# Kernel optimization log

Hardware: AMD Instinct MI355X
Metric: run time of the kernel (lower is better)

## Reference

```python
import jax, jax.numpy as jnp
import numpy as np

D = 768       # GATv2 in/out feats (num_heads=1)
D_OUT = 384   # fc output
K = 51        # round(top_rate * L) = round(0.1 * 512)
EPS = 1e-5    # nn.LayerNorm default eps


def _layer_norm(x, g, b):
    mu = jnp.mean(x, axis=-1, keepdims=True)
    var = jnp.mean((x - mu) ** 2, axis=-1, keepdims=True)
    return (x - mu) / jnp.sqrt(var + EPS) * g + b


def setup_inputs() -> dict:
    key = jax.random.key(0)
    ks = jax.random.split(key, 12)
    B, L = 4, 512
    s = 0.02
    return {
        "hidden_state": jax.random.normal(ks[0], (B, L, D), jnp.float32),
        "attention": jax.random.uniform(ks[1], (B, L, L), jnp.float32),
        # GATv2Conv params (fc_src, fc_dst, attn vector, output bias)
        "W_src": jax.random.normal(ks[2], (D, D), jnp.float32) * s,
        "b_src": jnp.zeros((D,), jnp.float32),
        "W_dst": jax.random.normal(ks[3], (D, D), jnp.float32) * s,
        "b_dst": jnp.zeros((D,), jnp.float32),
        "attn_vec": jax.random.normal(ks[4], (D,), jnp.float32) * s,
        "gat_bias": jnp.zeros((D,), jnp.float32),
        # GlobalAttentionPooling gate_nn: Linear(768, 1)
        "gate_W": jax.random.normal(ks[5], (D, 1), jnp.float32) * s,
        "gate_b": jnp.zeros((1,), jnp.float32),
        # LayerNorm(768)
        "ln_g": jnp.ones((D,), jnp.float32),
        "ln_b": jnp.zeros((D,), jnp.float32),
        # fc: Linear(768, 384)
        "fc_W": jax.random.normal(ks[6], (D, D_OUT), jnp.float32) * s,
        "fc_b": jnp.zeros((D_OUT,), jnp.float32),
        # LayerNorm(384)
        "ln2_g": jnp.ones((D_OUT,), jnp.float32),
        "ln2_b": jnp.zeros((D_OUT,), jnp.float32),
        "mask": jnp.ones((B, L), jnp.int32),  # unused by the original forward
        "type": 0,                              # unused string/type flag
    }


def reference(hidden_state, attention, W_src, b_src, W_dst, b_dst, attn_vec,
              gat_bias, gate_W, gate_b, ln_g, ln_b, fc_W, fc_b, ln2_g, ln2_b,
              mask, type):
    B, L, _ = hidden_state.shape
    # --- topk sparsification: each node i keeps K source neighbors ---
    vals, idx = jax.lax.top_k(attention, K)          # [B, L, K]
    valid = vals > 0.0                                # edges kept by pos_sign filter

    # --- GATv2Conv (num_heads=1, residual=Identity since 768==768) ---
    feat_src = hidden_state @ W_src + b_src           # [B, L, D]
    feat_dst = hidden_state @ W_dst + b_dst           # [B, L, D]
    g = feat_src[jnp.arange(B)[:, None, None], idx]   # [B, L, K, D] gathered src feats
    e = jax.nn.leaky_relu(g + feat_dst[:, :, None, :], 0.2)
    scores = jnp.einsum("blkd,d->blk", e, attn_vec)   # [B, L, K]
    scores = jnp.where(valid, scores, -1e9)           # removed edges masked out
    a = jax.nn.softmax(scores, axis=-1)               # edge_softmax per dst node
    h = jnp.einsum("blk,blkd->bld", a, g)             # weighted scatter-sum
    h = h + hidden_state + gat_bias                   # residual (identity) + bias
    h = jax.nn.leaky_relu(h, 0.01)                    # nn.LeakyReLU activation

    # --- GlobalAttentionPooling: softmax(gate) weighted segment reduce ---
    gate = h @ gate_W + gate_b                        # [B, L, 1]
    p = jax.nn.softmax(gate, axis=1)
    pooled = jnp.sum(p * h, axis=1)                   # [B, D]

    # --- head: fc(dropout(ln(relu(out)))) then ln2 (dropout = eval identity) ---
    out = _layer_norm(jax.nn.relu(pooled), ln_g, ln_b)
    out = out @ fc_W + fc_b
    out = _layer_norm(out, ln2_g, ln2_b)
    return out
```

## Files before the change

### kernel.cpp

```cpp
#include <hip/hip_runtime.h>
#include <math.h>

#define D 768
#define DOUT 384
#define LSEQ 512
#define BATCH 4
#define KTOP 51
#define EPS 1e-5f

typedef unsigned short ushort_t;
typedef __bf16 bf16x8 __attribute__((ext_vector_type(8)));
typedef float f32x4 __attribute__((ext_vector_type(4)));

#define GLOAD16(gp, lp)                                                        \
    __builtin_amdgcn_global_load_lds(                                          \
        (const __attribute__((address_space(1))) unsigned int*)(gp),           \
        (__attribute__((address_space(3))) unsigned int*)(lp), 16, 0, 0)

__device__ __forceinline__ ushort_t f2bf(float f) {
    unsigned int u = __builtin_bit_cast(unsigned int, f);
    u = (u + 0x7FFFu + ((u >> 16) & 1u)) >> 16;
    return (ushort_t)u;
}

__device__ __forceinline__ float bf2f(ushort_t u) {
    unsigned int v = ((unsigned int)u) << 16;
    return __builtin_bit_cast(float, v);
}

__global__ __launch_bounds__(256) void prep_kernel(const float* __restrict__ hidden,
                                                   ushort_t* __restrict__ Ah,
                                                   const float* __restrict__ W0,
                                                   const float* __restrict__ W1,
                                                   ushort_t* __restrict__ WT0,
                                                   ushort_t* __restrict__ WT1,
                                                   float* __restrict__ pooled,
                                                   float* __restrict__ z) {
    __shared__ float tile[32][33];
    const int bid = blockIdx.x;
    const int tid = threadIdx.x;
    if (bid < 1536) {
        const int i = (bid * 256 + tid) * 4;
        const float4 v = *(const float4*)(hidden + i);
        ushort4 o;
        o.x = f2bf(v.x); o.y = f2bf(v.y); o.z = f2bf(v.z); o.w = f2bf(v.w);
        *(ushort4*)(Ah + i) = o;
    } else if (bid < 2688) {
        const int t = bid - 1536;
        const int zz = t / 576;
        const int rem = t - zz * 576;
        const int by = rem / 24, bx = rem - by * 24;
        const float* W = zz ? W1 : W0;
        ushort_t* WT = zz ? WT1 : WT0;
        const int kbase = by * 32;
        const int nbase = bx * 32;
        const int r = tid >> 3, c4 = (tid & 7) * 4;

        const float4 v = *(const float4*)(W + (size_t)(kbase + r) * D + nbase + c4);
        tile[r][c4 + 0] = v.x; tile[r][c4 + 1] = v.y;
        tile[r][c4 + 2] = v.z; tile[r][c4 + 3] = v.w;
        __syncthreads();
        ushort4 o;
        o.x = f2bf(tile[c4 + 0][r]); o.y = f2bf(tile[c4 + 1][r]);
        o.z = f2bf(tile[c4 + 2][r]); o.w = f2bf(tile[c4 + 3][r]);
        *(ushort4*)(WT + (size_t)(nbase + r) * D + kbase + c4) = o;
    } else {
        for (int i = tid; i < BATCH * D; i += 256) pooled[i] = 0.f;
        for (int i = tid; i < BATCH * DOUT; i += 256) z[i] = 0.f;
    }
}

__global__ __launch_bounds__(256) void feat_gemm_kernel(const ushort_t* __restrict__ Ah,
                                                        const ushort_t* __restrict__ WT0,
                                                        const float* __restrict__ b0,
                                                        ushort_t* __restrict__ Csrc_bf,
                                                        const ushort_t* __restrict__ WT1,
                                                        const float* __restrict__ b1,
                                                        float* __restrict__ Cdst) {
    const ushort_t* WT = blockIdx.z ? WT1 : WT0;
    const float* bias = blockIdx.z ? b1 : b0;

    __shared__ ushort_t As[64 * 64];
    __shared__ ushort_t Bs[64 * 64];

    const int tid = threadIdx.x;
    const int lane = tid & 63;
    const int wave = tid >> 6;
    const int quad = lane >> 4;
    const int m15 = lane & 15;
    const int qRow = (wave & 1) * 32;
    const int qCol = (wave >> 1) * 32;

    const int rowBase = blockIdx.y * 64;
    const int colBase = blockIdx.x * 64;

    const int e0 = tid * 8;
    const int r0 = e0 >> 6;
    const int c0 = e0 & 63;
    const int cc = c0 >> 3;
    const int csw = (cc ^ (r0 & 7)) << 3;
    const ushort_t* Abase = Ah + (size_t)rowBase * D;
    const ushort_t* Bbase = WT + (size_t)colBase * D;

    f32x4 acc[2][2] = {};

    for (int kk = 0; kk < D; kk += 64) {
        __syncthreads();
        GLOAD16(Abase + (size_t)r0 * D + kk + csw, &As[e0]);
        GLOAD16(Abase + (size_t)(r0 + 32) * D + kk + csw, &As[e0 + 2048]);
        GLOAD16(Bbase + (size_t)r0 * D + kk + csw, &Bs[e0]);
        GLOAD16(Bbase + (size_t)(r0 + 32) * D + kk + csw, &Bs[e0 + 2048]);
        __syncthreads();

        bf16x8 a[2][2], b[2][2];
#pragma unroll
        for (int i = 0; i < 2; ++i) {
            const int row = qRow + i * 16 + m15;
            const int sw = row & 7;
#pragma unroll
            for (int ks = 0; ks < 2; ++ks)
                a[i][ks] = *(const bf16x8*)&As[row * 64 + ((((ks << 2) + quad) ^ sw) << 3)];
        }
#pragma unroll
        for (int j = 0; j < 2; ++j) {
            const int row = qCol + j * 16 + m15;
            const int sw = row & 7;
#pragma unroll
            for (int ks = 0; ks < 2; ++ks)
                b[j][ks] = *(const bf16x8*)&Bs[row * 64 + ((((ks << 2) + quad) ^ sw) << 3)];
        }
#pragma unroll
        for (int ks = 0; ks < 2; ++ks)
#pragma unroll
            for (int i = 0; i < 2; ++i)
#pragma unroll
                for (int j = 0; j < 2; ++j)
                    acc[i][j] = __builtin_amdgcn_mfma_f32_16x16x32_bf16(a[i][ks], b[j][ks], acc[i][j], 0, 0, 0);
    }

    if (blockIdx.z == 0) {
#pragma unroll
        for (int j = 0; j < 2; ++j) {
            const int col = colBase + qCol + j * 16 + m15;
            const float bv = bias[col];
#pragma unroll
            for (int i = 0; i < 2; ++i) {
                ushort_t* Cp = Csrc_bf + (size_t)(rowBase + qRow + i * 16 + quad * 4) * D + col;
#pragma unroll
                for (int r = 0; r < 4; ++r)
                    Cp[(size_t)r * D] = f2bf(acc[i][j][r] + bv);
            }
        }
    } else {
#pragma unroll
        for (int j = 0; j < 2; ++j) {
            const int col = colBase + qCol + j * 16 + m15;
            const float bv = bias[col];
#pragma unroll
            for (int i = 0; i < 2; ++i) {
                float* Cp = Cdst + (size_t)(rowBase + qRow + i * 16 + quad * 4) * D + col;
#pragma unroll
                for (int r = 0; r < 4; ++r)
                    Cp[(size_t)r * D] = acc[i][j][r] + bv;
            }
        }
    }
}

__global__ __launch_bounds__(256) void scoregath_kernel(const float* __restrict__ attn,
                                                        const ushort_t* __restrict__ fsrc_bf,
                                                        const float* __restrict__ feat_dst,
                                                        const float* __restrict__ attn_vec,
                                                        const float* __restrict__ gat_bias,
                                                        const float* __restrict__ hidden,
                                                        const float* __restrict__ gate_W,
                                                        const float* __restrict__ gate_b,
                                                        ushort_t* __restrict__ h,
                                                        float* __restrict__ gate) {
    const int row = blockIdx.x;
    const int b = row >> 9;
    const int tid = threadIdx.x;
    const int lane = tid & 63;
    const int wave = tid >> 6;

    __shared__ float vals[LSEQ];
    __shared__ float cval[320];
    __shared__ int   cidx[320];
    __shared__ int   nhi, outSlot;
    __shared__ int   kid[KTOP];
    __shared__ float kvv[KTOP];
    __shared__ float wm[4], wl[4];
    __shared__ float hpart[4][D];
    __shared__ float gred[4];

    if (tid == 0) { nhi = 0; outSlot = 0; }

    const float* a = attn + (size_t)row * LSEQ;
    const float v0 = a[tid];
    const float v1 = a[tid + 256];
    vals[tid] = v0;
    vals[tid + 256] = v1;
    __syncthreads();

    if (v0 > 0.75f) {
        const int s = atomicAdd(&nhi, 1);
        if (s < 320) { cval[s] = v0; cidx[s] = tid; }
    }
    if (v1 > 0.75f) {
        const int s = atomicAdd(&nhi, 1);
        if (s < 320) { cval[s] = v1; cidx[s] = tid + 256; }
    }
    __syncthreads();

    const int n = nhi;
    if (n >= KTOP && n <= 320) {
        if (tid < n) {
            const float v = cval[tid];
            const int e = cidx[tid];
            int r = 0;
            for (int j = 0; j < n; ++j) {
                const float u = cval[j];
                r += (u > v) || (u == v && cidx[j] < e);
            }
            if (r < KTOP) {
                const int s = atomicAdd(&outSlot, 1);
                kid[s] = e; kvv[s] = v;
            }
        }
    } else {
#pragma unroll
        for (int e0 = 0; e0 < 2; ++e0) {
            const int e = tid + e0 * 256;
            const float v = vals[e];
            int r = 0;
            for (int j = 0; j < LSEQ; ++j) {
                const float u = vals[j];
                r += (u > v) || (u == v && j < e);
            }
            if (r < KTOP) {
                const int s = atomicAdd(&outSlot, 1);
                kid[s] = e; kvv[s] = v;
            }
        }
    }

    const int d0 = lane * 8;
    const int d1 = 512 + lane * 4;
    const float* fdp = feat_dst + (size_t)row * D;
    float fdr[12], avr[12];
    {
        const float4 f0 = *(const float4*)(fdp + d0);
        const float4 f1 = *(const float4*)(fdp + d0 + 4);
        const float4 f2 = *(const float4*)(fdp + d1);
        const float4 a0 = *(const float4*)(attn_vec + d0);
        const float4 a1 = *(const float4*)(attn_vec + d0 + 4);
        const float4 a2 = *(const float4*)(attn_vec + d1);
        fdr[0]=f0.x; fdr[1]=f0.y; fdr[2]=f0.z;  fdr[3]=f0.w;
        fdr[4]=f1.x; fdr[5]=f1.y; fdr[6]=f1.z;  fdr[7]=f1.w;
        fdr[8]=f2.x; fdr[9]=f2.y; fdr[10]=f2.z; fdr[11]=f2.w;
        avr[0]=a0.x; avr[1]=a0.y; avr[2]=a0.z;  avr[3]=a0.w;
        avr[4]=a1.x; avr[5]=a1.y; avr[6]=a1.z;  avr[7]=a1.w;
        avr[8]=a2.x; avr[9]=a2.y; avr[10]=a2.z; avr[11]=a2.w;
    }
    __syncthreads();

    const ushort_t* fb = fsrc_bf + ((size_t)(b << 9)) * D;
    float m_run = -3.0e38f, l_run = 0.f;
    float acc[12] = {};
    for (int k = wave; k < KTOP; k += 4) {
        const ushort_t* g = fb + (size_t)kid[k] * D;
        const bf16x8 g0 = *(const bf16x8*)(g + d0);
        const ushort4 g1 = *(const ushort4*)(g + d1);

        float gf[12];
#pragma unroll
        for (int jj = 0; jj < 8; ++jj) gf[jj] = (float)g0[jj];
        gf[8] = bf2f(g1.x); gf[9] = bf2f(g1.y);
        gf[10] = bf2f(g1.z); gf[11] = bf2f(g1.w);

        float s = 0.f;
#pragma unroll
        for (int jj = 0; jj < 12; ++jj) {
            float x = gf[jj] + fdr[jj];
            x = x > 0.f ? x : 0.2f * x;
            s += x * avr[jj];
        }
#pragma unroll
        for (int off = 32; off > 0; off >>= 1) s += __shfl_xor(s, off);
        s = (kvv[k] > 0.f) ? s : -1e9f;

        if (s > m_run + 8.f) {
            const float rs = __expf(m_run - s);
            l_run *= rs;
#pragma unroll
            for (int jj = 0; jj < 12; ++jj) acc[jj] *= rs;
            m_run = s;
        }
        const float p = __expf(s - m_run);
        l_run += p;
#pragma unroll
        for (int jj = 0; jj < 12; ++jj) acc[jj] += p * gf[jj];
    }

    if (lane == 0) { wm[wave] = m_run; wl[wave] = l_run; }
    *(float4*)&hpart[wave][d0]     = *(float4*)&acc[0];
    *(float4*)&hpart[wave][d0 + 4] = *(float4*)&acc[4];
    *(float4*)&hpart[wave][d1]     = *(float4*)&acc[8];
    __syncthreads();

    const float M = fmaxf(fmaxf(wm[0], wm[1]), fmaxf(wm[2], wm[3]));
    const float r0 = __expf(wm[0] - M), r1 = __expf(wm[1] - M);
    const float r2 = __expf(wm[2] - M), r3 = __expf(wm[3] - M);
    const float invL = 1.f / (r0 * wl[0] + r1 * wl[1] + r2 * wl[2] + r3 * wl[3]);

    float dotp = 0.f;
    const float* hid = hidden + (size_t)row * D;
    ushort_t* hb = h + (size_t)row * D;
#pragma unroll
    for (int j = 0; j < 3; ++j) {
        const int d = tid + j * 256;
        const float hv = (r0 * hpart[0][d] + r1 * hpart[1][d] +
                          r2 * hpart[2][d] + r3 * hpart[3][d]) * invL;
        float v = hv + hid[d] + gat_bias[d];
        v = v > 0.f ? v : 0.01f * v;
        hb[d] = f2bf(v);
        dotp += v * gate_W[d];
    }
#pragma unroll
    for (int off = 32; off > 0; off >>= 1) dotp += __shfl_xor(dotp, off);
    if (lane == 0) gred[wave] = dotp;
    __syncthreads();
    if (tid == 0) gate[row] = gate_b[0] + gred[0] + gred[1] + gred[2] + gred[3];
}

__global__ __launch_bounds__(256) void pool_kernel(const ushort_t* __restrict__ h,
                                                   const float* __restrict__ gate,
                                                   float* __restrict__ pooled) {
    const int b = blockIdx.z;
    const int lbase = blockIdx.y * 64;
    const int d = blockIdx.x * 256 + threadIdx.x;
    const int tid = threadIdx.x;
    const int lane = tid & 63;
    const int w = tid >> 6;

    __shared__ float wred[4];
    __shared__ float ps[64];

    const float g0 = gate[b * LSEQ + tid];
    const float g1 = gate[b * LSEQ + tid + 256];
    float m = fmaxf(g0, g1);
#pragma unroll
    for (int off = 32; off > 0; off >>= 1) m = fmaxf(m, __shfl_xor(m, off));
    if (lane == 0) wred[w] = m;
    __syncthreads();
    m = fmaxf(fmaxf(wred[0], wred[1]), fmaxf(wred[2], wred[3]));
    float e = __expf(g0 - m) + __expf(g1 - m);
#pragma unroll
    for (int off = 32; off > 0; off >>= 1) e += __shfl_xor(e, off);
    __syncthreads();
    if (lane == 0) wred[w] = e;
    __syncthreads();
    const float inv = 1.f / (wred[0] + wred[1] + wred[2] + wred[3]);
    if (tid < 64) ps[tid] = __expf(gate[b * LSEQ + lbase + tid] - m) * inv;
    __syncthreads();

    const ushort_t* hb = h + ((size_t)(b * LSEQ + lbase)) * D + d;
    float acc = 0.f;
#pragma unroll 8
    for (int l = 0; l < 64; ++l) {
        acc += ps[l] * bf2f(hb[(size_t)l * D]);
    }
    atomicAdd(&pooled[b * D + d], acc);
}

__global__ __launch_bounds__(256) void fc_kernel(const float* __restrict__ pooled,
                                                 const float* __restrict__ ln_g,
                                                 const float* __restrict__ ln_b,
                                                 const float* __restrict__ fc_W,
                                                 float* __restrict__ z) {
    const int b = blockIdx.z;
    const int by = blockIdx.y;
    const int dbase = by * 256;
    const int jbase = blockIdx.x * 64;
    const int tid = threadIdx.x;
    const int lane = tid & 63;
    const int w = tid >> 6;
    const int jt = tid & 63;
    const int sub = tid >> 6;

    __shared__ float wred[4];
    __shared__ float ys[256];
    __shared__ float part[4][64];

    float v[3];
#pragma unroll
    for (int i = 0; i < 3; ++i) v[i] = fmaxf(pooled[b * D + tid + i * 256], 0.f);

    float s = v[0] + v[1] + v[2];
#pragma unroll
    for (int off = 32; off > 0; off >>= 1) s += __shfl_xor(s, off);
    if (lane == 0) wred[w] = s;
    __syncthreads();
    const float mu = (wred[0] + wred[1] + wred[2] + wred[3]) / (float)D;
    float vs = 0.f;
#pragma unroll
    for (int i = 0; i < 3; ++i) { const float dd = v[i] - mu; vs += dd * dd; }
#pragma unroll
    for (int off = 32; off > 0; off >>= 1) vs += __shfl_xor(vs, off);
    __syncthreads();
    if (lane == 0) wred[w] = vs;
    __syncthreads();
    const float rstd = rsqrtf((wred[0] + wred[1] + wred[2] + wred[3]) / (float)D + EPS);

    const float vb = (by == 0) ? v[0] : (by == 1 ? v[1] : v[2]);
    ys[tid] = (vb - mu) * rstd * ln_g[dbase + tid] + ln_b[dbase + tid];
    __syncthreads();

    const float* W = fc_W + (size_t)(dbase + sub * 64) * DOUT + jbase + jt;
    const float* yy = ys + sub * 64;
    float acc = 0.f;
#pragma unroll 8
    for (int i = 0; i < 64; ++i) {
        acc += yy[i] * W[(size_t)i * DOUT];
    }
    part[sub][jt] = acc;
    __syncthreads();
    if (sub == 0) {
        const float tot = part[0][jt] + part[1][jt] + part[2][jt] + part[3][jt];
        atomicAdd(&z[b * DOUT + jbase + jt], tot);
    }
}

__global__ __launch_bounds__(384) void ln2_kernel(const float* __restrict__ z,
                                                  const float* __restrict__ fc_b,
                                                  const float* __restrict__ ln2_g,
                                                  const float* __restrict__ ln2_b,
                                                  float* __restrict__ out) {
    const int b = blockIdx.x;
    const int tid = threadIdx.x;
    const int lane = tid & 63;
    const int wave = tid >> 6;
    __shared__ float wred[6];

    const float v = z[b * DOUT + tid] + fc_b[tid];

    float s = v;
#pragma unroll
    for (int off = 32; off > 0; off >>= 1) s += __shfl_xor(s, off);
    if (lane == 0) wred[wave] = s;
    __syncthreads();
    float mu = 0.f;
#pragma unroll
    for (int w = 0; w < 6; ++w) mu += wred[w];
    mu /= (float)DOUT;
    __syncthreads();

    const float dd = v - mu;
    float s2 = dd * dd;
#pragma unroll
    for (int off = 32; off > 0; off >>= 1) s2 += __shfl_xor(s2, off);
    if (lane == 0) wred[wave] = s2;
    __syncthreads();
    float var = 0.f;
#pragma unroll
    for (int w = 0; w < 6; ++w) var += wred[w];
    const float rstd = rsqrtf(var / (float)DOUT + EPS);

    out[b * DOUT + tid] = dd * rstd * ln2_g[tid] + ln2_b[tid];
}

extern "C" void kernel_launch(void* const* d_in, const int* in_sizes, int n_in,
                              void* d_out, int out_size, void* d_ws, size_t ws_size,
                              hipStream_t stream) {
    const float* hidden   = (const float*)d_in[0];
    const float* attention= (const float*)d_in[1];
    const float* W_src    = (const float*)d_in[2];
    const float* b_src    = (const float*)d_in[3];
    const float* W_dst    = (const float*)d_in[4];
    const float* b_dst    = (const float*)d_in[5];
    const float* attn_vec = (const float*)d_in[6];
    const float* gat_bias = (const float*)d_in[7];
    const float* gate_W   = (const float*)d_in[8];
    const float* gate_b   = (const float*)d_in[9];
    const float* ln_g     = (const float*)d_in[10];
    const float* ln_b     = (const float*)d_in[11];
    const float* fc_W     = (const float*)d_in[12];
    const float* fc_b     = (const float*)d_in[13];
    const float* ln2_g    = (const float*)d_in[14];
    const float* ln2_b    = (const float*)d_in[15];
    float* out = (float*)d_out;

    const int M = BATCH * LSEQ;
    float* feat_dst = (float*)d_ws;
    float* gate     = feat_dst + (size_t)M * D;
    float* pooled   = gate + M;
    float* z        = pooled + BATCH * D;
    ushort_t* Ah    = (ushort_t*)(z + BATCH * DOUT);
    ushort_t* WT0   = Ah + (size_t)M * D;
    ushort_t* WT1   = WT0 + (size_t)D * D;
    ushort_t* fsrcb = WT1 + (size_t)D * D;
    ushort_t* h     = fsrcb + (size_t)M * D;

    hipLaunchKernelGGL(prep_kernel, dim3(2689), dim3(256), 0, stream,
                       hidden, Ah, W_src, W_dst, WT0, WT1, pooled, z);
    hipLaunchKernelGGL(feat_gemm_kernel, dim3(D / 64, M / 64, 2), dim3(256), 0, stream,
                       Ah, WT0, b_src, fsrcb, WT1, b_dst, feat_dst);
    hipLaunchKernelGGL(scoregath_kernel, dim3(M), dim3(256), 0, stream,
                       attention, fsrcb, feat_dst, attn_vec, gat_bias, hidden,
                       gate_W, gate_b, h, gate);
    hipLaunchKernelGGL(pool_kernel, dim3(D / 256, LSEQ / 64, BATCH), dim3(256), 0, stream,
                       h, gate, pooled);
    hipLaunchKernelGGL(fc_kernel, dim3(DOUT / 64, D / 256, BATCH), dim3(256), 0, stream,
                       pooled, ln_g, ln_b, fc_W, z);
    hipLaunchKernelGGL(ln2_kernel, dim3(BATCH), dim3(384), 0, stream,
                       z, fc_b, ln2_g, ln2_b, out);
}
```

Before: 153.9 us.

## Enlarge GEMM row tile and drop atomics in pooling and fc reductions

The feature GEMM now uses 128x64 tiles with each wave computing 64x32, which raises A/B reuse per block and halves the number of blocks. The pool and fc kernels stop splitting the reduction dimension across blocks. Each block now reduces the full sequence or feature range and writes its result directly instead of using atomicAdd, which also removes the zero-init blocks from prep_kernel. The cost is far fewer blocks in pool (12) and fc (24), and longer serial loops per thread, which may underuse the GPU.

```diff
diff --git a/kernel.cpp b/kernel.cpp
--- a/kernel.cpp
+++ b/kernel.cpp
@@ -33,9 +33,7 @@
                                                    const float* __restrict__ W0,
                                                    const float* __restrict__ W1,
                                                    ushort_t* __restrict__ WT0,
-                                                   ushort_t* __restrict__ WT1,
-                                                   float* __restrict__ pooled,
-                                                   float* __restrict__ z) {
+                                                   ushort_t* __restrict__ WT1) {
     __shared__ float tile[32][33];
     const int bid = blockIdx.x;
     const int tid = threadIdx.x;
@@ -45,7 +43,7 @@
         ushort4 o;
         o.x = f2bf(v.x); o.y = f2bf(v.y); o.z = f2bf(v.z); o.w = f2bf(v.w);
         *(ushort4*)(Ah + i) = o;
-    } else if (bid < 2688) {
+    } else {
         const int t = bid - 1536;
         const int zz = t / 576;
         const int rem = t - zz * 576;
@@ -64,9 +62,6 @@
         o.x = f2bf(tile[c4 + 0][r]); o.y = f2bf(tile[c4 + 1][r]);
         o.z = f2bf(tile[c4 + 2][r]); o.w = f2bf(tile[c4 + 3][r]);
         *(ushort4*)(WT + (size_t)(nbase + r) * D + kbase + c4) = o;
-    } else {
-        for (int i = tid; i < BATCH * D; i += 256) pooled[i] = 0.f;
-        for (int i = tid; i < BATCH * DOUT; i += 256) z[i] = 0.f;
     }
 }
 
@@ -80,7 +75,7 @@
     const ushort_t* WT = blockIdx.z ? WT1 : WT0;
     const float* bias = blockIdx.z ? b1 : b0;
 
-    __shared__ ushort_t As[64 * 64];
+    __shared__ ushort_t As[128 * 64];
     __shared__ ushort_t Bs[64 * 64];
 
     const int tid = threadIdx.x;
@@ -88,10 +83,10 @@
     const int wave = tid >> 6;
     const int quad = lane >> 4;
     const int m15 = lane & 15;
-    const int qRow = (wave & 1) * 32;
-    const int qCol = (wave >> 1) * 32;
-
-    const int rowBase = blockIdx.y * 64;
+    const int wr = (wave >> 1) * 64;
+    const int wc = (wave & 1) * 32;
+
+    const int rowBase = blockIdx.y * 128;
     const int colBase = blockIdx.x * 64;
 
     const int e0 = tid * 8;
@@ -102,20 +97,22 @@
     const ushort_t* Abase = Ah + (size_t)rowBase * D;
     const ushort_t* Bbase = WT + (size_t)colBase * D;
 
-    f32x4 acc[2][2] = {};
+    f32x4 acc[4][2] = {};
 
     for (int kk = 0; kk < D; kk += 64) {
         __syncthreads();
-        GLOAD16(Abase + (size_t)r0 * D + kk + csw, &As[e0]);
-        GLOAD16(Abase + (size_t)(r0 + 32) * D + kk + csw, &As[e0 + 2048]);
-        GLOAD16(Bbase + (size_t)r0 * D + kk + csw, &Bs[e0]);
-        GLOAD16(Bbase + (size_t)(r0 + 32) * D + kk + csw, &Bs[e0 + 2048]);
+        GLOAD16(Abase + (size_t)r0 * D + kk + csw,         &As[e0]);
+        GLOAD16(Abase + (size_t)(r0 + 32) * D + kk + csw,  &As[e0 + 2048]);
+        GLOAD16(Abase + (size_t)(r0 + 64) * D + kk + csw,  &As[e0 + 4096]);
+        GLOAD16(Abase + (size_t)(r0 + 96) * D + kk + csw,  &As[e0 + 6144]);
+        GLOAD16(Bbase + (size_t)r0 * D + kk + csw,         &Bs[e0]);
+        GLOAD16(Bbase + (size_t)(r0 + 32) * D + kk + csw,  &Bs[e0 + 2048]);
         __syncthreads();
 
-        bf16x8 a[2][2], b[2][2];
-#pragma unroll
-        for (int i = 0; i < 2; ++i) {
-            const int row = qRow + i * 16 + m15;
+        bf16x8 a[4][2], b[2][2];
+#pragma unroll
+        for (int i = 0; i < 4; ++i) {
+            const int row = wr + i * 16 + m15;
             const int sw = row & 7;
 #pragma unroll
             for (int ks = 0; ks < 2; ++ks)
@@ -123,7 +120,7 @@
         }
 #pragma unroll
         for (int j = 0; j < 2; ++j) {
-            const int row = qCol + j * 16 + m15;
+            const int row = wc + j * 16 + m15;
             const int sw = row & 7;
 #pragma unroll
             for (int ks = 0; ks < 2; ++ks)
@@ -132,7 +129,7 @@
 #pragma unroll
         for (int ks = 0; ks < 2; ++ks)
 #pragma unroll
-            for (int i = 0; i < 2; ++i)
+            for (int i = 0; i < 4; ++i)
 #pragma unroll
                 for (int j = 0; j < 2; ++j)
                     acc[i][j] = __builtin_amdgcn_mfma_f32_16x16x32_bf16(a[i][ks], b[j][ks], acc[i][j], 0, 0, 0);
@@ -141,11 +138,11 @@
     if (blockIdx.z == 0) {
 #pragma unroll
         for (int j = 0; j < 2; ++j) {
-            const int col = colBase + qCol + j * 16 + m15;
+            const int col = colBase + wc + j * 16 + m15;
             const float bv = bias[col];
 #pragma unroll
-            for (int i = 0; i < 2; ++i) {
-                ushort_t* Cp = Csrc_bf + (size_t)(rowBase + qRow + i * 16 + quad * 4) * D + col;
+            for (int i = 0; i < 4; ++i) {
+                ushort_t* Cp = Csrc_bf + (size_t)(rowBase + wr + i * 16 + quad * 4) * D + col;
 #pragma unroll
                 for (int r = 0; r < 4; ++r)
                     Cp[(size_t)r * D] = f2bf(acc[i][j][r] + bv);
@@ -154,11 +151,11 @@
     } else {
 #pragma unroll
         for (int j = 0; j < 2; ++j) {
-            const int col = colBase + qCol + j * 16 + m15;
+            const int col = colBase + wc + j * 16 + m15;
             const float bv = bias[col];
 #pragma unroll
-            for (int i = 0; i < 2; ++i) {
-                float* Cp = Cdst + (size_t)(rowBase + qRow + i * 16 + quad * 4) * D + col;
+            for (int i = 0; i < 4; ++i) {
+                float* Cp = Cdst + (size_t)(rowBase + wr + i * 16 + quad * 4) * D + col;
 #pragma unroll
                 for (int r = 0; r < 4; ++r)
                     Cp[(size_t)r * D] = acc[i][j][r] + bv;
@@ -336,15 +333,14 @@
 __global__ __launch_bounds__(256) void pool_kernel(const ushort_t* __restrict__ h,
                                                    const float* __restrict__ gate,
                                                    float* __restrict__ pooled) {
-    const int b = blockIdx.z;
-    const int lbase = blockIdx.y * 64;
+    const int b = blockIdx.y;
     const int d = blockIdx.x * 256 + threadIdx.x;
     const int tid = threadIdx.x;
     const int lane = tid & 63;
     const int w = tid >> 6;
 
     __shared__ float wred[4];
-    __shared__ float ps[64];
+    __shared__ float ps[LSEQ];
 
     const float g0 = gate[b * LSEQ + tid];
     const float g1 = gate[b * LSEQ + tid + 256];
@@ -361,16 +357,20 @@
     if (lane == 0) wred[w] = e;
     __syncthreads();
     const float inv = 1.f / (wred[0] + wred[1] + wred[2] + wred[3]);
-    if (tid < 64) ps[tid] = __expf(gate[b * LSEQ + lbase + tid] - m) * inv;
-    __syncthreads();
-
-    const ushort_t* hb = h + ((size_t)(b * LSEQ + lbase)) * D + d;
-    float acc = 0.f;
-#pragma unroll 8
-    for (int l = 0; l < 64; ++l) {
-        acc += ps[l] * bf2f(hb[(size_t)l * D]);
-    }
-    atomicAdd(&pooled[b * D + d], acc);
+    ps[tid] = __expf(g0 - m) * inv;
+    ps[tid + 256] = __expf(g1 - m) * inv;
+    __syncthreads();
+
+    const ushort_t* hb = h + (size_t)(b * LSEQ) * D + d;
+    float a0 = 0.f, a1 = 0.f, a2 = 0.f, a3 = 0.f;
+#pragma unroll 4
+    for (int l = 0; l < LSEQ; l += 4) {
+        a0 += ps[l + 0] * bf2f(hb[(size_t)(l + 0) * D]);
+        a1 += ps[l + 1] * bf2f(hb[(size_t)(l + 1) * D]);
+        a2 += ps[l + 2] * bf2f(hb[(size_t)(l + 2) * D]);
+        a3 += ps[l + 3] * bf2f(hb[(size_t)(l + 3) * D]);
+    }
+    pooled[b * D + d] = (a0 + a1) + (a2 + a3);
 }
 
 __global__ __launch_bounds__(256) void fc_kernel(const float* __restrict__ pooled,
@@ -378,9 +378,7 @@
                                                  const float* __restrict__ ln_b,
                                                  const float* __restrict__ fc_W,
                                                  float* __restrict__ z) {
-    const int b = blockIdx.z;
-    const int by = blockIdx.y;
-    const int dbase = by * 256;
+    const int b = blockIdx.y;
     const int jbase = blockIdx.x * 64;
     const int tid = threadIdx.x;
     const int lane = tid & 63;
@@ -389,7 +387,7 @@
     const int sub = tid >> 6;
 
     __shared__ float wred[4];
-    __shared__ float ys[256];
+    __shared__ float ys[D];
     __shared__ float part[4][64];
 
     float v[3];
@@ -412,22 +410,25 @@
     __syncthreads();
     const float rstd = rsqrtf((wred[0] + wred[1] + wred[2] + wred[3]) / (float)D + EPS);
 
-    const float vb = (by == 0) ? v[0] : (by == 1 ? v[1] : v[2]);
-    ys[tid] = (vb - mu) * rstd * ln_g[dbase + tid] + ln_b[dbase + tid];
-    __syncthreads();
-
-    const float* W = fc_W + (size_t)(dbase + sub * 64) * DOUT + jbase + jt;
-    const float* yy = ys + sub * 64;
+#pragma unroll
+    for (int i = 0; i < 3; ++i) {
+        const int dd = tid + i * 256;
+        ys[dd] = (v[i] - mu) * rstd * ln_g[dd] + ln_b[dd];
+    }
+    __syncthreads();
+
+    const float* W = fc_W + (size_t)(sub * 192) * DOUT + jbase + jt;
+    const float* yy = ys + sub * 192;
     float acc = 0.f;
 #pragma unroll 8
-    for (int i = 0; i < 64; ++i) {
+    for (int i = 0; i < 192; ++i) {
         acc += yy[i] * W[(size_t)i * DOUT];
     }
     part[sub][jt] = acc;
     __syncthreads();
     if (sub == 0) {
-        const float tot = part[0][jt] + part[1][jt] + part[2][jt] + part[3][jt];
-        atomicAdd(&z[b * DOUT + jbase + jt], tot);
+        z[b * DOUT + jbase + jt] =
+            (part[0][jt] + part[1][jt]) + (part[2][jt] + part[3][jt]);
     }
 }
 
@@ -501,16 +502,16 @@
     ushort_t* fsrcb = WT1 + (size_t)D * D;
     ushort_t* h     = fsrcb + (size_t)M * D;
 
-    hipLaunchKernelGGL(prep_kernel, dim3(2689), dim3(256), 0, stream,
-                       hidden, Ah, W_src, W_dst, WT0, WT1, pooled, z);
-    hipLaunchKernelGGL(feat_gemm_kernel, dim3(D / 64, M / 64, 2), dim3(256), 0, stream,
+    hipLaunchKernelGGL(prep_kernel, dim3(2688), dim3(256), 0, stream,
+                       hidden, Ah, W_src, W_dst, WT0, WT1);
+    hipLaunchKernelGGL(feat_gemm_kernel, dim3(D / 64, M / 128, 2), dim3(256), 0, stream,
                        Ah, WT0, b_src, fsrcb, WT1, b_dst, feat_dst);
     hipLaunchKernelGGL(scoregath_kernel, dim3(M), dim3(256), 0, stream,
                        attention, fsrcb, feat_dst, attn_vec, gat_bias, hidden,
                        gate_W, gate_b, h, gate);
-    hipLaunchKernelGGL(pool_kernel, dim3(D / 256, LSEQ / 64, BATCH), dim3(256), 0, stream,
+    hipLaunchKernelGGL(pool_kernel, dim3(D / 256, BATCH), dim3(256), 0, stream,
                        h, gate, pooled);
-    hipLaunchKernelGGL(fc_kernel, dim3(DOUT / 64, D / 256, BATCH), dim3(256), 0, stream,
+    hipLaunchKernelGGL(fc_kernel, dim3(DOUT / 64, BATCH), dim3(256), 0, stream,
                        pooled, ln_g, ln_b, fc_W, z);
     hipLaunchKernelGGL(ln2_kernel, dim3(BATCH), dim3(384), 0, stream,
                        z, fc_b, ln2_g, ln2_b, out);
```

New measurement: 172.8 us. 1.12x slower.
